# Kernel optimization log

Hardware: AMD Instinct MI355X
Metric: run time of the kernel (lower is better)

The kernel has to match this reference:

```python
import jax, jax.numpy as jnp
import numpy as np

EMBED_DIM = 1024
N_HEADS = 16
HEAD_DIM = EMBED_DIM // N_HEADS


def setup_inputs() -> dict:
    key = jax.random.key(0)
    ks = jax.random.split(key, 5)
    B, T, C = 4, 2048, EMBED_DIM
    s = 0.02
    return {
        "x": jax.random.normal(ks[0], (B, T, C), dtype=jnp.float32),
        "w_qkv": jax.random.normal(ks[1], (C, 3 * C), dtype=jnp.float32) * s,
        "b_qkv": jnp.zeros((3 * C,), dtype=jnp.float32),
        "w_proj": jax.random.normal(ks[2], (C, C), dtype=jnp.float32) * s,
        "b_proj": jnp.zeros((C,), dtype=jnp.float32),
    }


def reference(x, w_qkv, b_qkv, w_proj, b_proj):
    B, T, C = x.shape
    H, D = N_HEADS, HEAD_DIM
    qkv = x @ w_qkv + b_qkv  # [B,T,3C]
    q, k, v = jnp.split(qkv, 3, axis=-1)
    # [B,H,T,D]
    q = q.reshape(B, T, H, D).transpose(0, 2, 1, 3)
    k = k.reshape(B, T, H, D).transpose(0, 2, 1, 3)
    v = v.reshape(B, T, H, D).transpose(0, 2, 1, 3)
    scale = jnp.asarray(D, x.dtype) ** -0.5
    att = jnp.einsum("bhqd,bhkd->bhqk", q, k) * scale  # [B,H,T,T]
    causal = jnp.tril(jnp.ones((T, T), dtype=bool))
    att = jnp.where(causal, att, jnp.asarray(-jnp.inf, att.dtype))
    att = jax.nn.softmax(att, axis=-1)
    out = jnp.einsum("bhqk,bhkd->bhqd", att, v)  # [B,H,T,D]
    out = out.transpose(0, 2, 1, 3).reshape(B, T, C)
    return out @ w_proj + b_proj
```

## Files before the change

### kernel.cpp

```cpp
#include <hip/hip_runtime.h>
#include <hip/hip_bf16.h>


typedef __bf16 bf16x8 __attribute__((ext_vector_type(8)));
typedef float f32x4 __attribute__((ext_vector_type(4)));
typedef unsigned short u16x8 __attribute__((ext_vector_type(8)));
typedef unsigned short u16x4 __attribute__((ext_vector_type(4)));
typedef unsigned int u32;

#define LOG2E 1.44269504088896340736f
#define NEG_INF (-__builtin_inff())

#define AS_GLOBAL(p) ((const __attribute__((address_space(1))) u32*)(p))
#define AS_LDS(p) ((__attribute__((address_space(3))) u32*)(p))

__device__ __forceinline__ unsigned short f2bf(float f) {
  unsigned int u = __builtin_bit_cast(unsigned int, f);
  u += 0x7fff + ((u >> 16) & 1);
  return (unsigned short)(u >> 16);
}

__device__ __forceinline__ u32 cvt_pk_bf16(float lo, float hi) {
  u32 r;
  asm("v_cvt_pk_bf16_f32 %0, %1, %2" : "=v"(r) : "v"(lo), "v"(hi));
  return r;
}

__device__ __forceinline__ bf16x8 ld_frag(const unsigned short* p) {
  return __builtin_bit_cast(bf16x8, *reinterpret_cast<const u16x8*>(p));
}

__global__ void k_convert(const float* __restrict__ in, unsigned short* __restrict__ out, int n4) {
  int i = blockIdx.x * blockDim.x + threadIdx.x;
  int stride = gridDim.x * blockDim.x;
  for (; i < n4; i += stride) {
    float4 v = reinterpret_cast<const float4*>(in)[i];
    u16x4 o = { f2bf(v.x), f2bf(v.y), f2bf(v.z), f2bf(v.w) };
    reinterpret_cast<u16x4*>(out)[i] = o;
  }
}

__global__ void k_transpose(const float* __restrict__ in, unsigned short* __restrict__ out,
                            int K, int N, int scaleN, float scl) {
  __shared__ float tile[32][33];
  int n0 = blockIdx.x * 32, k0 = blockIdx.y * 32;
  int tx = threadIdx.x & 31, ty = threadIdx.x >> 5;
#pragma unroll
  for (int i = 0; i < 4; i++)
    tile[ty + i * 8][tx] = in[(size_t)(k0 + ty + i * 8) * N + n0 + tx];
  __syncthreads();
#pragma unroll
  for (int i = 0; i < 4; i++) {
    int n = n0 + ty + i * 8;
    float v = tile[tx][ty + i * 8];
    if (n < scaleN) v *= scl;
    out[(size_t)n * K + k0 + tx] = f2bf(v);
  }
}

__global__ void k_scale_bias(const float* __restrict__ in, float* __restrict__ out,
                             int n, int scaleN, float scl) {
  int i = blockIdx.x * blockDim.x + threadIdx.x;
  if (i < n) out[i] = (i < scaleN) ? in[i] * scl : in[i];
}

template <bool BF16_OUT>
__global__ __launch_bounds__(256) void k_gemm(
    const unsigned short* __restrict__ A, const unsigned short* __restrict__ Bt,
    const float* __restrict__ bias, void* __restrict__ Cv, int M, int N, int K) {
  constexpr int BK = 64;
  __shared__ unsigned short Asm[128][BK];
  __shared__ unsigned short Bsm[128][BK];
  const int tid = threadIdx.x;
  const int lane = tid & 63, w = tid >> 6;
  const int wr = w >> 1, wc = w & 1;
  const int brow = blockIdx.x * 128, bcol = blockIdx.y * 128;
  const int r0 = lane & 15, kq = lane >> 4;

  f32x4 acc[4][4] = {};

  const int srow = lane >> 3, scol = (lane & 7) * 8;

  for (int k0 = 0; k0 < K; k0 += BK) {
    __syncthreads();
#pragma unroll
    for (int q = 0; q < 4; q++) {
      int c = w * 4 + q;
      const unsigned short* ga = &A[(size_t)(brow + c * 8 + srow) * K + k0 + scol];
      const unsigned short* gb = &Bt[(size_t)(bcol + c * 8 + srow) * K + k0 + scol];
      __builtin_amdgcn_global_load_lds(AS_GLOBAL(ga), AS_LDS(&Asm[c * 8][0]), 16, 0, 0);
      __builtin_amdgcn_global_load_lds(AS_GLOBAL(gb), AS_LDS(&Bsm[c * 8][0]), 16, 0, 0);
    }
    __syncthreads();
#pragma unroll
    for (int c = 0; c < 2; c++) {
      bf16x8 af[4], bfr[4];
#pragma unroll
      for (int m = 0; m < 4; m++)
        af[m] = ld_frag(&Asm[wr * 64 + m * 16 + r0][c * 32 + kq * 8]);
#pragma unroll
      for (int n = 0; n < 4; n++)
        bfr[n] = ld_frag(&Bsm[wc * 64 + n * 16 + r0][c * 32 + kq * 8]);
      __builtin_amdgcn_s_setprio(1);
#pragma unroll
      for (int m = 0; m < 4; m++)
#pragma unroll
        for (int n = 0; n < 4; n++)
          acc[m][n] = __builtin_amdgcn_mfma_f32_16x16x32_bf16(af[m], bfr[n], acc[m][n], 0, 0, 0);
      __builtin_amdgcn_s_setprio(0);
    }
  }

  const int orow = kq * 4;
#pragma unroll
  for (int n = 0; n < 4; n++) {
#pragma unroll
    for (int m = 0; m < 4; m++) {
      int col = bcol + wc * 64 + n * 16 + r0;
      float bv = bias[col];
#pragma unroll
      for (int r = 0; r < 4; r++) {
        int row = brow + wr * 64 + m * 16 + orow + r;
        float v = acc[m][n][r] + bv;
        if (BF16_OUT)
          ((unsigned short*)Cv)[(size_t)row * N + col] = f2bf(v);
        else
          ((float*)Cv)[(size_t)row * N + col] = v;
      }
    }
  }
}

__global__ __launch_bounds__(256, 3) void k_flash(const unsigned short* __restrict__ qkv,
                                                  unsigned short* __restrict__ att, int T) {
  constexpr int C3 = 3072, C = 1024;
  __shared__ unsigned short Ksm[2][64][72];
  __shared__ unsigned short Vsm[2][64][72];

  const int tid = threadIdx.x, lane = tid & 63, w = tid >> 6;
  const int bh = blockIdx.x;
  const int qtp = gridDim.y - 1 - blockIdx.y;
  const int b = bh >> 4, h = bh & 15;
  const int q0 = qtp * 128;
  const int r0 = lane & 15, kq = lane >> 4;

  const size_t rowbase = (size_t)b * T * C3;
  const int qb0 = q0 + w * 32, qb1 = qb0 + 16;

  bf16x8 qf[2][2];
  {
    const unsigned short* qp0 = &qkv[rowbase + (size_t)(qb0 + r0) * C3 + h * 64];
    qf[0][0] = ld_frag(&qp0[kq * 8]);
    qf[0][1] = ld_frag(&qp0[32 + kq * 8]);
    const unsigned short* qp1 = qp0 + (size_t)16 * C3;
    qf[1][0] = ld_frag(&qp1[kq * 8]);
    qf[1][1] = ld_frag(&qp1[32 + kq * 8]);
  }

  f32x4 accO[2][4] = {};
  f32x4 ls4[2] = {{0.f,0.f,0.f,0.f},{0.f,0.f,0.f,0.f}};
  float m_run[2] = {NEG_INF, NEG_INF};

  const int stk = tid >> 3, sd8 = (tid & 7) * 8;
  const unsigned short* kbase = &qkv[rowbase + (size_t)stk * C3 + h * 64 + sd8 + C];
  constexpr size_t PSTRIDE = (size_t)32 * C3;

  u16x8 kreg[2], vreg[2];
  auto LOADT = [&](size_t off) {
#pragma unroll
    for (int p = 0; p < 2; p++) {
      kreg[p] = *reinterpret_cast<const u16x8*>(kbase + off + p * PSTRIDE);
      vreg[p] = *reinterpret_cast<const u16x8*>(kbase + off + p * PSTRIDE + C);
    }
  };
  auto WRITET = [&](int buf) {
#pragma unroll
    for (int p = 0; p < 2; p++) {
      int tkk = p * 32 + stk;
      *reinterpret_cast<u16x8*>(&Ksm[buf][tkk][sd8]) = kreg[p];
      int tkx = tkk ^ sd8;
#pragma unroll
      for (int i = 0; i < 8; i++) Vsm[buf][sd8 + i][tkx] = vreg[p][i];
    }
  };

  auto TILE = [&](int buf, int k0) {
    if (k0 > qb1 + 15) return;
    const unsigned short(*Ks)[72] = Ksm[buf];
    const unsigned short(*Vs)[72] = Vsm[buf];

    f32x4 st[2][4];
    __builtin_amdgcn_s_setprio(1);
#pragma unroll
    for (int s = 0; s < 4; s++) {
      bf16x8 kf0 = ld_frag(&Ks[s * 16 + r0][kq * 8]);
      bf16x8 kf1 = ld_frag(&Ks[s * 16 + r0][32 + kq * 8]);
#pragma unroll
      for (int u = 0; u < 2; u++) {
        f32x4 a = {};
        a = __builtin_amdgcn_mfma_f32_16x16x32_bf16(kf0, qf[u][0], a, 0, 0, 0);
        a = __builtin_amdgcn_mfma_f32_16x16x32_bf16(kf1, qf[u][1], a, 0, 0, 0);
        st[u][s] = a;
      }
    }
    __builtin_amdgcn_s_setprio(0);

    u32 pd[2][2][4];
#pragma unroll
    for (int u = 0; u < 2; u++) {
      const int qbu = u ? qb1 : qb0;
      const int qmy = qbu + r0;
      f32x4 sv[4];
      if (k0 + 63 > qbu) {
#pragma unroll
        for (int s = 0; s < 4; s++)
#pragma unroll
          for (int r = 0; r < 4; r++) {
            int kg = k0 + s * 16 + kq * 4 + r;
            sv[s][r] = (kg > qmy) ? NEG_INF : st[u][s][r];
          }
      } else {
#pragma unroll
        for (int s = 0; s < 4; s++) sv[s] = st[u][s];
      }

      f32x4 m4 = __builtin_elementwise_max(__builtin_elementwise_max(sv[0], sv[1]),
                                           __builtin_elementwise_max(sv[2], sv[3]));
      float mx = fmaxf(fmaxf(m4[0], m4[1]), fmaxf(m4[2], m4[3]));

      if (__any(mx > m_run[u] + 8.f)) {
        mx = fmaxf(mx, __shfl_xor(mx, 16));
        mx = fmaxf(mx, __shfl_xor(mx, 32));
        float mn = fmaxf(m_run[u], mx);
        float corr = exp2f(m_run[u] - mn);
        m_run[u] = mn;
        ls4[u] *= corr;
        float cq[4];
#pragma unroll
        for (int r = 0; r < 4; r++) cq[r] = __shfl(corr, kq * 4 + r);
#pragma unroll
        for (int n = 0; n < 4; n++)
#pragma unroll
          for (int r = 0; r < 4; r++) accO[u][n][r] *= cq[r];
      }

#pragma unroll
      for (int s = 0; s < 4; s++) {
        f32x4 d = sv[s] - m_run[u];
        f32x4 p = { exp2f(d[0]), exp2f(d[1]), exp2f(d[2]), exp2f(d[3]) };
        sv[s] = p;
        ls4[u] += p;
      }
      pd[u][0][0] = cvt_pk_bf16(sv[0][0], sv[0][1]);
      pd[u][0][1] = cvt_pk_bf16(sv[0][2], sv[0][3]);
      pd[u][0][2] = cvt_pk_bf16(sv[1][0], sv[1][1]);
      pd[u][0][3] = cvt_pk_bf16(sv[1][2], sv[1][3]);
      pd[u][1][0] = cvt_pk_bf16(sv[2][0], sv[2][1]);
      pd[u][1][1] = cvt_pk_bf16(sv[2][2], sv[2][3]);
      pd[u][1][2] = cvt_pk_bf16(sv[3][0], sv[3][1]);
      pd[u][1][3] = cvt_pk_bf16(sv[3][2], sv[3][3]);
    }

    __builtin_amdgcn_s_setprio(1);
#pragma unroll
    for (int t = 0; t < 2; t++) {
      bf16x8 pa0 = __builtin_bit_cast(bf16x8, *reinterpret_cast<u16x8*>(pd[0][t]));
      bf16x8 pa1 = __builtin_bit_cast(bf16x8, *reinterpret_cast<u16x8*>(pd[1][t]));
#pragma unroll
      for (int n = 0; n < 4; n++) {
        int d = n * 16 + r0;
        int swzb = d & 56;
        const u16x4 lo = *reinterpret_cast<const u16x4*>(&Vs[d][(t * 32 + kq * 4) ^ swzb]);
        const u16x4 hi = *reinterpret_cast<const u16x4*>(&Vs[d][(t * 32 + 16 + kq * 4) ^ swzb]);
        u16x8 vbw;
#pragma unroll
        for (int i = 0; i < 4; i++) { vbw[i] = lo[i]; vbw[4 + i] = hi[i]; }
        bf16x8 vb = __builtin_bit_cast(bf16x8, vbw);
        accO[0][n] = __builtin_amdgcn_mfma_f32_16x16x32_bf16(pa0, vb, accO[0][n], 0, 0, 0);
        accO[1][n] = __builtin_amdgcn_mfma_f32_16x16x32_bf16(pa1, vb, accO[1][n], 0, 0, 0);
      }
    }
    __builtin_amdgcn_s_setprio(0);
  };

  int buf = 0;
  LOADT(0);
  WRITET(0);
  size_t koff = (size_t)64 * C3;
  const int nkt = (q0 + 128) >> 6;
  for (int kt = 0; kt < nkt - 1; kt++) {
    __syncthreads();
    LOADT(koff);
    koff += (size_t)64 * C3;
    TILE(buf, kt * 64);
    WRITET(buf ^ 1);
    buf ^= 1;
  }
  __syncthreads();
  TILE(buf, (nkt - 1) * 64);

#pragma unroll
  for (int u = 0; u < 2; u++) {
    const int qbu = u ? qb1 : qb0;
    float l = ls4[u][0] + ls4[u][1] + ls4[u][2] + ls4[u][3];
    l += __shfl_xor(l, 16);
    l += __shfl_xor(l, 32);
    float lr[4];
#pragma unroll
    for (int r = 0; r < 4; r++) lr[r] = 1.f / __shfl(l, kq * 4 + r);
#pragma unroll
    for (int n = 0; n < 4; n++) {
#pragma unroll
      for (int r = 0; r < 4; r++) {
        int qrow = qbu + kq * 4 + r;
        float v = accO[u][n][r] * lr[r];
        att[((size_t)b * T + qrow) * C + h * 64 + n * 16 + r0] = f2bf(v);
      }
    }
  }
}

extern "C" void kernel_launch(void* const* d_in, const int* in_sizes, int n_in,
                              void* d_out, int out_size, void* d_ws, size_t ws_size,
                              hipStream_t stream) {
  const float* x = (const float*)d_in[0];
  const float* w_qkv = (const float*)d_in[1];
  const float* b_qkv = (const float*)d_in[2];
  const float* w_proj = (const float*)d_in[3];
  const float* b_proj = (const float*)d_in[4];

  constexpr int B = 4, T = 2048, C = 1024, C3 = 3072;
  constexpr int M = B * T;
  constexpr float SCL = 0.125f * LOG2E;

  unsigned short* x_bf = (unsigned short*)d_ws;
  unsigned short* wqkvT = x_bf + (size_t)M * C;
  unsigned short* wprojT = wqkvT + (size_t)C3 * C;
  unsigned short* qkv = wprojT + (size_t)C * C;
  unsigned short* att = qkv + (size_t)M * C3;
  float* bias_s = (float*)(att + (size_t)M * C);

  hipLaunchKernelGGL(k_convert, dim3(2048), dim3(256), 0, stream, x, x_bf, M * C / 4);
  hipLaunchKernelGGL(k_transpose, dim3(C3 / 32, C / 32), dim3(256), 0, stream,
                     w_qkv, wqkvT, C, C3, C, SCL);
  hipLaunchKernelGGL(k_transpose, dim3(C / 32, C / 32), dim3(256), 0, stream,
                     w_proj, wprojT, C, C, 0, 1.f);
  hipLaunchKernelGGL(k_scale_bias, dim3((C3 + 255) / 256), dim3(256), 0, stream,
                     b_qkv, bias_s, C3, C, SCL);
  hipLaunchKernelGGL((k_gemm<true>), dim3(M / 128, C3 / 128), dim3(256), 0, stream,
                     x_bf, wqkvT, bias_s, (void*)qkv, M, C3, C);
  hipLaunchKernelGGL(k_flash, dim3(64, 16), dim3(256), 0, stream, qkv, att, T);
  hipLaunchKernelGGL((k_gemm<false>), dim3(M / 128, C / 128), dim3(256), 0, stream,
                     att, wprojT, b_proj, d_out, M, C, C);
}
```

Measured before the change: 180.4 us.

## Software-pipeline GEMM with double-buffered swizzled LDS and fine-grained barriers

Rewrites the projection GEMM main loop as an 8-phase software pipeline. Global-to-LDS loads for future K-slices are issued while MFMAs run on already-resident fragments, using a double-buffered LDS split into 32-wide K halves with an XOR swizzle to avoid bank conflicts. The two full __syncthreads per tile are replaced by partial vmcnt waits plus barriers. The intent is to hide global load latency and LDS conflicts behind matrix math, at the cost of more LDS, more complex scheduling and reliance on exact vmcnt counting for correctness.

```diff
diff --git a/kernel.cpp b/kernel.cpp
--- a/kernel.cpp
+++ b/kernel.cpp
@@ -64,51 +64,102 @@
   if (i < n) out[i] = (i < scaleN) ? in[i] * scl : in[i];
 }
 
+#define GVMCNT4 asm volatile("s_waitcnt vmcnt(4)")
+#define GBAR { __builtin_amdgcn_s_barrier(); __builtin_amdgcn_sched_barrier(0); }
+#define MFMA8(MB, AF, BF) \
+  { __builtin_amdgcn_s_setprio(1); \
+    _Pragma("unroll") for (int n_ = 0; n_ < 4; ++n_) { \
+      acc[MB][n_]     = __builtin_amdgcn_mfma_f32_16x16x32_bf16(AF[0], BF[n_], acc[MB][n_], 0, 0, 0); \
+      acc[MB + 1][n_] = __builtin_amdgcn_mfma_f32_16x16x32_bf16(AF[1], BF[n_], acc[MB + 1][n_], 0, 0, 0); \
+    } __builtin_amdgcn_s_setprio(0); }
+
 template <bool BF16_OUT>
-__global__ __launch_bounds__(256) void k_gemm(
+__global__ __launch_bounds__(256, 2) void k_gemm(
     const unsigned short* __restrict__ A, const unsigned short* __restrict__ Bt,
     const float* __restrict__ bias, void* __restrict__ Cv, int M, int N, int K) {
-  constexpr int BK = 64;
-  __shared__ unsigned short Asm[128][BK];
-  __shared__ unsigned short Bsm[128][BK];
+  __shared__ unsigned short Asm[2][2][128][32];
+  __shared__ unsigned short Bsm[2][2][128][32];
   const int tid = threadIdx.x;
   const int lane = tid & 63, w = tid >> 6;
   const int wr = w >> 1, wc = w & 1;
   const int brow = blockIdx.x * 128, bcol = blockIdx.y * 128;
   const int r0 = lane & 15, kq = lane >> 4;
+  const int rswz = (r0 >> 2) & 3;
+  const int rdslot = (kq ^ rswz) * 8;
+
+  const int srow = w * 32 + (lane >> 2);
+  const int sslot = ((lane & 3) ^ ((lane >> 4) & 3)) * 8;
+  const unsigned short* aSrc = A + (size_t)(brow + srow) * K + sslot;
+  const unsigned short* bSrc = Bt + (size_t)(bcol + srow) * K + sslot;
 
   f32x4 acc[4][4] = {};
-
-  const int srow = lane >> 3, scol = (lane & 7) * 8;
-
-  for (int k0 = 0; k0 < K; k0 += BK) {
-    __syncthreads();
-#pragma unroll
-    for (int q = 0; q < 4; q++) {
-      int c = w * 4 + q;
-      const unsigned short* ga = &A[(size_t)(brow + c * 8 + srow) * K + k0 + scol];
-      const unsigned short* gb = &Bt[(size_t)(bcol + c * 8 + srow) * K + k0 + scol];
-      __builtin_amdgcn_global_load_lds(AS_GLOBAL(ga), AS_LDS(&Asm[c * 8][0]), 16, 0, 0);
-      __builtin_amdgcn_global_load_lds(AS_GLOBAL(gb), AS_LDS(&Bsm[c * 8][0]), 16, 0, 0);
-    }
-    __syncthreads();
-#pragma unroll
-    for (int c = 0; c < 2; c++) {
-      bf16x8 af[4], bfr[4];
-#pragma unroll
-      for (int m = 0; m < 4; m++)
-        af[m] = ld_frag(&Asm[wr * 64 + m * 16 + r0][c * 32 + kq * 8]);
-#pragma unroll
-      for (int n = 0; n < 4; n++)
-        bfr[n] = ld_frag(&Bsm[wc * 64 + n * 16 + r0][c * 32 + kq * 8]);
-      __builtin_amdgcn_s_setprio(1);
-#pragma unroll
-      for (int m = 0; m < 4; m++)
-#pragma unroll
-        for (int n = 0; n < 4; n++)
-          acc[m][n] = __builtin_amdgcn_mfma_f32_16x16x32_bf16(af[m], bfr[n], acc[m][n], 0, 0, 0);
-      __builtin_amdgcn_s_setprio(0);
-    }
+  const int NT = K >> 6;
+
+#define STAGEA(BUF, KH, TS)                                                              \
+  { int kc_ = (TS) * 64 + (KH) * 32;                                                     \
+    __builtin_amdgcn_global_load_lds(AS_GLOBAL(aSrc + kc_), AS_LDS(&Asm[BUF][KH][w * 32][0]), 16, 0, 0); \
+    __builtin_amdgcn_global_load_lds(AS_GLOBAL(aSrc + kc_ + (size_t)16 * K), AS_LDS(&Asm[BUF][KH][w * 32 + 16][0]), 16, 0, 0); }
+#define STAGEB(BUF, KH, TS)                                                              \
+  { int kc_ = (TS) * 64 + (KH) * 32;                                                     \
+    __builtin_amdgcn_global_load_lds(AS_GLOBAL(bSrc + kc_), AS_LDS(&Bsm[BUF][KH][w * 32][0]), 16, 0, 0); \
+    __builtin_amdgcn_global_load_lds(AS_GLOBAL(bSrc + kc_ + (size_t)16 * K), AS_LDS(&Bsm[BUF][KH][w * 32 + 16][0]), 16, 0, 0); }
+#define LDA(BUF, KH, MM) ld_frag(&Asm[BUF][KH][wr * 64 + (MM) * 16 + r0][rdslot])
+#define LDB(BUF, KH, NN) ld_frag(&Bsm[BUF][KH][wc * 64 + (NN) * 16 + r0][rdslot])
+
+  STAGEA(0, 0, 0); STAGEB(0, 0, 0); STAGEA(0, 1, 0); STAGEB(0, 1, 0); STAGEA(1, 0, 1);
+  __syncthreads();
+
+  bf16x8 afA[2], afB[2], bfE[4], bfO[4];
+  afA[0] = LDA(0, 0, 0); afA[1] = LDA(0, 0, 1);
+#pragma unroll
+  for (int n = 0; n < 4; ++n) bfE[n] = LDB(0, 0, n);
+
+  const int NIT = NT >> 1;
+  for (int it = 0; it < NIT; ++it) {
+    const int t1 = 2 * it + 1, t2 = 2 * it + 2, t3 = 2 * it + 3;
+    const bool g2 = (t2 < NT), g3 = (t3 < NT);
+    afB[0] = LDA(0, 0, 2); afB[1] = LDA(0, 0, 3);
+    STAGEB(1, 0, t1);
+    MFMA8(0, afA, bfE);
+    GVMCNT4; GBAR;
+    afA[0] = LDA(0, 1, 0); afA[1] = LDA(0, 1, 1);
+#pragma unroll
+    for (int n = 0; n < 4; ++n) bfO[n] = LDB(0, 1, n);
+    STAGEA(1, 1, t1);
+    MFMA8(2, afB, bfE);
+    GVMCNT4; GBAR;
+    afB[0] = LDA(0, 1, 2); afB[1] = LDA(0, 1, 3);
+    STAGEB(1, 1, t1);
+    MFMA8(0, afA, bfO);
+    GVMCNT4; GBAR;
+    afA[0] = LDA(1, 0, 0); afA[1] = LDA(1, 0, 1);
+#pragma unroll
+    for (int n = 0; n < 4; ++n) bfE[n] = LDB(1, 0, n);
+    if (g2) STAGEA(0, 0, t2);
+    MFMA8(2, afB, bfO);
+    GVMCNT4; GBAR;
+    afB[0] = LDA(1, 0, 2); afB[1] = LDA(1, 0, 3);
+    if (g2) STAGEB(0, 0, t2);
+    MFMA8(0, afA, bfE);
+    GVMCNT4; GBAR;
+    afA[0] = LDA(1, 1, 0); afA[1] = LDA(1, 1, 1);
+#pragma unroll
+    for (int n = 0; n < 4; ++n) bfO[n] = LDB(1, 1, n);
+    if (g2) STAGEA(0, 1, t2);
+    MFMA8(2, afB, bfE);
+    GVMCNT4; GBAR;
+    afB[0] = LDA(1, 1, 2); afB[1] = LDA(1, 1, 3);
+    if (g2) STAGEB(0, 1, t2);
+    MFMA8(0, afA, bfO);
+    GVMCNT4; GBAR;
+    if (it + 1 < NIT) {
+      afA[0] = LDA(0, 0, 0); afA[1] = LDA(0, 0, 1);
+#pragma unroll
+      for (int n = 0; n < 4; ++n) bfE[n] = LDB(0, 0, n);
+    }
+    if (g3) STAGEA(1, 0, t3);
+    MFMA8(2, afB, bfO);
+    GVMCNT4; GBAR;
   }
 
   const int orow = kq * 4;
@@ -129,6 +180,10 @@
       }
     }
   }
+#undef STAGEA
+#undef STAGEB
+#undef LDA
+#undef LDB
 }
 
 __global__ __launch_bounds__(256, 3) void k_flash(const unsigned short* __restrict__ qkv,
```

Result: no change. 177.8 us (-1.5%).
